# Kernel optimization log

Hardware: AMD Instinct MI355X
Metric: run time of the kernel (lower is better)

The kernel has to match this reference:

```python
import jax, jax.numpy as jnp
import numpy as np

L, B, D_IN, LATENT, H_ODE = 50, 256, 256, 512, 1024
DT = 0.1  # uniform time increment per observation


def setup_inputs() -> dict:
    key = jax.random.key(0)
    ks = jax.random.split(key, 9)
    feat = jax.random.normal(ks[0], (L, B, D_IN), dtype=jnp.float32)
    tp = jnp.full((L, B, 1), DT, dtype=jnp.float32)
    data = jnp.concatenate([feat, tp], axis=-1)  # (L, B, D_IN+1)
    hid = 2 * LATENT  # GRUCell hidden size
    s_mlp1 = 1.0 / np.sqrt(LATENT)
    s_mlp2 = 1.0 / np.sqrt(H_ODE)
    s_gru_i = 1.0 / np.sqrt(hid)
    return {
        "data": data,
        # ODE func MLP: Linear(LATENT,H_ODE) -> tanh -> Linear(H_ODE,LATENT)
        "mlp_w1": jax.random.uniform(ks[1], (LATENT, H_ODE), jnp.float32, -s_mlp1, s_mlp1),
        "mlp_b1": jax.random.uniform(ks[2], (H_ODE,), jnp.float32, -s_mlp1, s_mlp1),
        "mlp_w2": jax.random.uniform(ks[3], (H_ODE, LATENT), jnp.float32, -s_mlp2, s_mlp2),
        "mlp_b2": jax.random.uniform(ks[4], (LATENT,), jnp.float32, -s_mlp2, s_mlp2),
        # GRUCell(D_IN, hid): torch layout W_ih (3*hid, D_IN), W_hh (3*hid, hid)
        "gru_wih": jax.random.uniform(ks[5], (3 * hid, D_IN), jnp.float32, -s_gru_i, s_gru_i),
        "gru_bih": jax.random.uniform(ks[6], (3 * hid,), jnp.float32, -s_gru_i, s_gru_i),
        "gru_whh": jax.random.uniform(ks[7], (3 * hid, hid), jnp.float32, -s_gru_i, s_gru_i),
        "gru_bhh": jax.random.uniform(ks[8], (3 * hid,), jnp.float32, -s_gru_i, s_gru_i),
    }


def reference(data, mlp_w1, mlp_b1, mlp_w2, mlp_b2, gru_wih, gru_bih, gru_whh, gru_bhh):
    x_seq = data[..., :-1]          # (L, B, D_IN)
    dt_seq = data[..., -1]          # (L, B) per-step time increments
    l, bs, _ = x_seq.shape
    latent = mlp_w1.shape[0]

    # With uniform dt, minimum_step = total/200 and each step uses
    # n_intermediate_tp = floor(200/L) linspace points -> n_sub Euler substeps.
    n_tp = max(2, 200 // l)
    n_sub = n_tp - 1

    def ode_f(y):
        return jnp.tanh(y @ mlp_w1 + mlp_b1) @ mlp_w2 + mlp_b2

    def gru_cell(x, h):
        gi = x @ gru_wih.T + gru_bih
        gh = h @ gru_whh.T + gru_bhh
        ir, iz, inn = jnp.split(gi, 3, axis=-1)
        hr, hz, hn = jnp.split(gh, 3, axis=-1)
        r = jax.nn.sigmoid(ir + hr)
        z = jax.nn.sigmoid(iz + hz)
        n = jnp.tanh(inn + r * hn)
        return (1.0 - z) * n + z * h

    def step(carry, inp):
        ode_state, gru_state, _ = carry
        x, dt = inp                      # x: (B, D_IN), dt: (B,)
        h_step = (dt / n_sub)[:, None]   # Euler substep size
        y = ode_state
        for _ in range(n_sub):           # fixed small unroll
            y = y + ode_f(y) * h_step
        new_h = gru_cell(x, jnp.concatenate([y, gru_state], axis=-1))
        # Original code: ode_state = new_h[..., :latent]; gru_state = new_h[..., :-latent]
        # (both are the first `latent` dims -- faithful to the source)
        new_ode = new_h[:, :latent]
        new_gru = new_h[:, :latent]
        return (new_ode, new_gru, new_h), new_ode

    zeros_lat = jnp.zeros((bs, latent), dtype=data.dtype)
    init = (zeros_lat, zeros_lat, jnp.zeros((bs, 2 * latent), dtype=data.dtype))
    (_, _, new_h), ode_states_post = jax.lax.scan(step, init, (x_seq, dt_seq))
    return ode_states_post, new_h
```

## Files before the change

kernel.cpp:

```cpp
#include <hip/hip_runtime.h>

#define LSEQ 50
#define BATCH 256
#define DIN 256
#define LAT 512
#define HID 1024
#define ROWSTRIDE 257
#define NBLK 256

typedef __attribute__((ext_vector_type(8))) short s16x8;
typedef __attribute__((ext_vector_type(4))) float f32x4;
using u16 = unsigned short;
using u64 = unsigned long long;

__device__ __forceinline__ u16 bfhi(float v) {
  union { float f; unsigned u; } a; a.f = v;
  return (u16)((a.u + 0x7FFFu + ((a.u >> 16) & 1u)) >> 16);
}
__device__ __forceinline__ void split2(float v, u16& h, u16& l) {
  u16 hu = bfhi(v);
  union { unsigned u; float f; } hf; hf.u = ((unsigned)hu) << 16;
  h = hu; l = bfhi(v - hf.f);
}
__device__ __forceinline__ float p2f(u16 h, u16 l) {
  union { unsigned u; float f; } a, b;
  a.u = ((unsigned)h) << 16; b.u = ((unsigned)l) << 16;
  return a.f + b.f;
}
__device__ __forceinline__ float sigmoidf_(float x) { return 1.f / (1.f + __expf(-x)); }
__device__ __forceinline__ f32x4 mfma16(s16x8 a, s16x8 b, f32x4 c) {
  return __builtin_amdgcn_mfma_f32_16x16x32_bf16(a, b, c, 0, 0, 0);
}
__device__ __forceinline__ ushort4 ldu4(const u16* p) { return *(const ushort4*)p; }
__device__ __forceinline__ void stu4(u16* p, ushort4 v) { *(ushort4*)p = v; }

__device__ __forceinline__ ushort4 ldu4c(const u16* p) {
  u64 v = __hip_atomic_load((const u64*)p, __ATOMIC_RELAXED, __HIP_MEMORY_SCOPE_AGENT);
  union { u64 q; ushort4 s; } u; u.q = v; return u.s;
}
__device__ __forceinline__ u16 ldu16c(const u16* p) {
  return __hip_atomic_load(p, __ATOMIC_RELAXED, __HIP_MEMORY_SCOPE_AGENT);
}
__device__ __forceinline__ void stu16c(u16* p, u16 v) {
  __hip_atomic_store(p, v, __ATOMIC_RELAXED, __HIP_MEMORY_SCOPE_AGENT);
}

__device__ __forceinline__ void slice_barrier(unsigned* line, unsigned k) {
  asm volatile("s_waitcnt vmcnt(0)" ::: "memory");
  __syncthreads();
  if (threadIdx.x == 0) {
    __hip_atomic_fetch_add(line, 1u, __ATOMIC_RELAXED, __HIP_MEMORY_SCOPE_AGENT);
    const unsigned tgt = k * 32u;
    while (__hip_atomic_load(line, __ATOMIC_RELAXED, __HIP_MEMORY_SCOPE_AGENT) < tgt) {
      __builtin_amdgcn_s_sleep(1);
    }
  }
  __syncthreads();
}

__global__ __launch_bounds__(256) void tsplit_k(const float* __restrict__ W,
    u16* __restrict__ Thi, u16* __restrict__ Tlo, int K, int N)
{
  __shared__ unsigned Ts[32][33];
  const int bk = blockIdx.x * 32, bn = blockIdx.y * 32;
  const int t = threadIdx.x;
  const int n_l = t & 31, k_l4 = (t >> 5) * 4;
  #pragma unroll
  for (int i = 0; i < 4; i++) {
    float v = W[(size_t)(bk + k_l4 + i) * N + bn + n_l];
    u16 h, l; split2(v, h, l);
    Ts[k_l4 + i][n_l] = ((unsigned)h << 16) | l;
  }
  __syncthreads();
  const int k_l = t & 31, n_l2 = t >> 5;
  #pragma unroll
  for (int i = 0; i < 4; i++) {
    int nn = n_l2 + 8 * i;
    unsigned u = Ts[k_l][nn];
    size_t o = (size_t)(bn + nn) * K + bk + k_l;
    Thi[o] = (u16)(u >> 16);
    Tlo[o] = (u16)(u & 0xFFFFu);
  }
}

__global__ __launch_bounds__(256) void esplit_k(const float* __restrict__ W,
    u16* __restrict__ Phi, u16* __restrict__ Plo)
{
  size_t i4 = ((size_t)blockIdx.x * 256 + threadIdx.x) * 4;
  float4 v = *(const float4*)&W[i4];
  u16 h[4], l[4];
  split2(v.x, h[0], l[0]); split2(v.y, h[1], l[1]);
  split2(v.z, h[2], l[2]); split2(v.w, h[3], l[3]);
  *(ushort4*)&Phi[i4] = make_ushort4(h[0], h[1], h[2], h[3]);
  *(ushort4*)&Plo[i4] = make_ushort4(l[0], l[1], l[2], l[3]);
}

__global__ __launch_bounds__(256) void init_k(u16* __restrict__ c0h, u16* __restrict__ c0l,
                                              unsigned* __restrict__ bar)
{
  size_t i4 = ((size_t)blockIdx.x * 256 + threadIdx.x) * 4;
  *(ushort4*)&c0h[i4] = make_ushort4(0, 0, 0, 0);
  *(ushort4*)&c0l[i4] = make_ushort4(0, 0, 0, 0);
  if (blockIdx.x == 0 && threadIdx.x < 16) bar[threadIdx.x * 64] = 0u;
}

template<int EPI, int NITER>
__device__ __forceinline__ void gemm_phase(
    u16* __restrict__ Sah, u16* __restrict__ Sal,
    u16* __restrict__ Sbh, u16* __restrict__ Sbl,
    const u16* __restrict__ Ahi, const u16* __restrict__ Alo, int ldA, int m0,
    const u16* __restrict__ Bhi, const u16* __restrict__ Blo, int ldB, int n0,
    const float* __restrict__ bias,
    u16* __restrict__ Ohi, u16* __restrict__ Olo,
    const float* __restrict__ data, int t, int tid)
{
  const int lane = tid & 63, wave = tid >> 6;
  const int wm = (wave >> 1) << 4, wn = (wave & 1) << 4;
  const int lr = lane & 15, lq = lane >> 4;
  const int srow = tid >> 3, sk4 = (tid & 7) << 2;
  const int sidx = srow * 40 + sk4;
  const size_t rowA = (size_t)(m0 + srow) * ldA + sk4;
  const size_t rowB = (size_t)(n0 + srow) * ldB + sk4;
  f32x4 acc = {0.f, 0.f, 0.f, 0.f};
  ushort4 rah[4], ral[4], rbh[4], rbl[4];
  #pragma unroll
  for (int d = 0; d < 4; ++d) {
    const int k0 = d << 5;
    rah[d] = ldu4c(&Ahi[rowA + k0]); ral[d] = ldu4c(&Alo[rowA + k0]);
    rbh[d] = ldu4(&Bhi[rowB + k0]);  rbl[d] = ldu4(&Blo[rowB + k0]);
  }
  #pragma unroll
  for (int d = 0; d < 4; ++d) {
    stu4(&Sah[d * 1280 + sidx], rah[d]); stu4(&Sal[d * 1280 + sidx], ral[d]);
    stu4(&Sbh[d * 1280 + sidx], rbh[d]); stu4(&Sbl[d * 1280 + sidx], rbl[d]);
  }
  __syncthreads();
  constexpr int NSEG = NITER / 4;
  for (int p = 0; p < NSEG; ++p) {
    const int rb = (p & 1) * 5120;
    const int wb = 5120 - rb;
    const bool pf = (p + 1 < NSEG);
    if (pf) {
      #pragma unroll
      for (int d = 0; d < 4; ++d) {
        const int k0 = (((p + 1) << 2) + d) << 5;
        rah[d] = ldu4c(&Ahi[rowA + k0]); ral[d] = ldu4c(&Alo[rowA + k0]);
        rbh[d] = ldu4(&Bhi[rowB + k0]);  rbl[d] = ldu4(&Blo[rowB + k0]);
      }
    }
    #pragma unroll
    for (int d = 0; d < 4; ++d) {
      const int fa = rb + d * 1280 + (wm + lr) * 40 + lq * 8;
      const int fb = rb + d * 1280 + (wn + lr) * 40 + lq * 8;
      s16x8 ah = *(const s16x8*)&Sah[fa];
      s16x8 al = *(const s16x8*)&Sal[fa];
      s16x8 bh = *(const s16x8*)&Sbh[fb];
      s16x8 bl = *(const s16x8*)&Sbl[fb];
      acc = mfma16(ah, bh, acc);
      acc = mfma16(ah, bl, acc);
      acc = mfma16(al, bh, acc);
    }
    if (pf) {
      #pragma unroll
      for (int d = 0; d < 4; ++d) {
        stu4(&Sah[wb + d * 1280 + sidx], rah[d]); stu4(&Sal[wb + d * 1280 + sidx], ral[d]);
        stu4(&Sbh[wb + d * 1280 + sidx], rbh[d]); stu4(&Sbl[wb + d * 1280 + sidx], rbl[d]);
      }
    }
    __syncthreads();
  }
  #pragma unroll
  for (int r = 0; r < 4; ++r) {
    const int row = m0 + wm + lq * 4 + r;
    const int col = n0 + wn + lr;
    float v = acc[r] + bias[col];
    size_t o = (size_t)row * HID + col;
    if (EPI == 1) {
      float h1 = tanhf(v);
      u16 h, l; split2(h1, h, l);
      stu16c(&Ohi[o], h); stu16c(&Olo[o], l);
    } else {
      float dt3 = data[(size_t)(t * BATCH + row) * ROWSTRIDE + DIN] * (1.f / 3.f);
      float y = p2f(ldu16c(&Ohi[o]), ldu16c(&Olo[o])) + v * dt3;
      u16 h, l; split2(y, h, l);
      stu16c(&Ohi[o], h); stu16c(&Olo[o], l);
    }
  }
}

template<bool PLANES>
__device__ __forceinline__ void gru_phase(
    u16* pool,
    const u16* __restrict__ chi, const u16* __restrict__ clo,
    const float* __restrict__ whh, const u16* __restrict__ whhh, const u16* __restrict__ whhl,
    const float* __restrict__ wih, const u16* __restrict__ wihh, const u16* __restrict__ wihl,
    const float* __restrict__ bih, const float* __restrict__ bhh,
    const float* __restrict__ data, int t,
    u16* __restrict__ nhi, u16* __restrict__ nlo,
    float* __restrict__ out, int g0, int m0, int tid)
{
  u16* sAh = pool;
  u16* sAl = pool + 5120;
  u16* sBh = pool + 10240;
  u16* sBl = pool + 25600;
  const int lane = tid & 63, wave = tid >> 6;
  const int wm = (wave >> 1) << 4, wn = (wave & 1) << 4;
  const int lr = lane & 15, lq = lane >> 4;
  const int srow = tid >> 3, sk4 = (tid & 7) << 2;
  const int sidx = srow * 40 + sk4;
  f32x4 aR = {0,0,0,0}, aZ = {0,0,0,0}, aNh = {0,0,0,0}, aNi = {0,0,0,0};

  ushort4 rah[2], ral[2], rbh[2][3], rbl[2][3];
  float4  rbf[2][3];
  float   rxf[2][4];

  {
    const size_t rowA = (size_t)(m0 + srow) * HID + sk4;
    #pragma unroll
    for (int j = 0; j < 2; ++j) {
      const int k0 = j << 5;
      rah[j] = ldu4c(&chi[rowA + k0]); ral[j] = ldu4c(&clo[rowA + k0]);
      #pragma unroll
      for (int g = 0; g < 3; ++g) {
        const size_t rr = (size_t)(g * 1024 + g0 + srow) * 1024 + k0 + sk4;
        if (PLANES) { rbh[j][g] = ldu4(&whhh[rr]); rbl[j][g] = ldu4(&whhl[rr]); }
        else rbf[j][g] = *(const float4*)&whh[rr];
      }
    }
    #pragma unroll
    for (int j = 0; j < 2; ++j) {
      stu4(&sAh[j * 1280 + sidx], rah[j]); stu4(&sAl[j * 1280 + sidx], ral[j]);
      #pragma unroll
      for (int g = 0; g < 3; ++g) {
        if (PLANES) {
          stu4(&sBh[j * 3840 + g * 1280 + sidx], rbh[j][g]);
          stu4(&sBl[j * 3840 + g * 1280 + sidx], rbl[j][g]);
        } else {
          float4 w4 = rbf[j][g];
          u16 h0,l0,h1,l1,h2,l2,h3,l3;
          split2(w4.x,h0,l0); split2(w4.y,h1,l1); split2(w4.z,h2,l2); split2(w4.w,h3,l3);
          stu4(&sBh[j * 3840 + g * 1280 + sidx], make_ushort4(h0,h1,h2,h3));
          stu4(&sBl[j * 3840 + g * 1280 + sidx], make_ushort4(l0,l1,l2,l3));
        }
      }
    }
    __syncthreads();
    for (int p = 0; p < 16; ++p) {
      const int rb = (p & 1) * 2;
      const int wb = 2 - rb;
      const bool pf = (p + 1 < 16);
      if (pf) {
        #pragma unroll
        for (int j = 0; j < 2; ++j) {
          const int k0 = (((p + 1) << 1) + j) << 5;
          rah[j] = ldu4c(&chi[rowA + k0]); ral[j] = ldu4c(&clo[rowA + k0]);
          #pragma unroll
          for (int g = 0; g < 3; ++g) {
            const size_t rr = (size_t)(g * 1024 + g0 + srow) * 1024 + k0 + sk4;
            if (PLANES) { rbh[j][g] = ldu4(&whhh[rr]); rbl[j][g] = ldu4(&whhl[rr]); }
            else rbf[j][g] = *(const float4*)&whh[rr];
          }
        }
      }
      #pragma unroll
      for (int j = 0; j < 2; ++j) {
        const int sa = (rb + j) * 1280 + (wm + lr) * 40 + lq * 8;
        const int sb = (rb + j) * 3840 + (wn + lr) * 40 + lq * 8;
        s16x8 ah = *(const s16x8*)&sAh[sa];
        s16x8 al = *(const s16x8*)&sAl[sa];
        #pragma unroll
        for (int g = 0; g < 3; ++g) {
          s16x8 bh = *(const s16x8*)&sBh[sb + g * 1280];
          s16x8 bl = *(const s16x8*)&sBl[sb + g * 1280];
          f32x4 c = (g == 0) ? aR : (g == 1) ? aZ : aNh;
          c = mfma16(ah, bh, c); c = mfma16(ah, bl, c); c = mfma16(al, bh, c);
          if (g == 0) aR = c; else if (g == 1) aZ = c; else aNh = c;
        }
      }
      if (pf) {
        #pragma unroll
        for (int j = 0; j < 2; ++j) {
          stu4(&sAh[(wb + j) * 1280 + sidx], rah[j]); stu4(&sAl[(wb + j) * 1280 + sidx], ral[j]);
          #pragma unroll
          for (int g = 0; g < 3; ++g) {
            if (PLANES) {
              stu4(&sBh[(wb + j) * 3840 + g * 1280 + sidx], rbh[j][g]);
              stu4(&sBl[(wb + j) * 3840 + g * 1280 + sidx], rbl[j][g]);
            } else {
              float4 w4 = rbf[j][g];
              u16 h0,l0,h1,l1,h2,l2,h3,l3;
              split2(w4.x,h0,l0); split2(w4.y,h1,l1); split2(w4.z,h2,l2); split2(w4.w,h3,l3);
              stu4(&sBh[(wb + j) * 3840 + g * 1280 + sidx], make_ushort4(h0,h1,h2,h3));
              stu4(&sBl[(wb + j) * 3840 + g * 1280 + sidx], make_ushort4(l0,l1,l2,l3));
            }
          }
        }
      }
      __syncthreads();
    }
  }

  {
    const size_t rowX = (size_t)(t * BATCH + m0 + srow) * ROWSTRIDE + sk4;
    #pragma unroll
    for (int j = 0; j < 2; ++j) {
      const int k0 = j << 5;
      #pragma unroll
      for (int i = 0; i < 4; ++i) rxf[j][i] = data[rowX + k0 + i];
      #pragma unroll
      for (int g = 0; g < 3; ++g) {
        const size_t rr = (size_t)(g * 1024 + g0 + srow) * 256 + k0 + sk4;
        if (PLANES) { rbh[j][g] = ldu4(&wihh[rr]); rbl[j][g] = ldu4(&wihl[rr]); }
        else rbf[j][g] = *(const float4*)&wih[rr];
      }
    }
    #pragma unroll
    for (int j = 0; j < 2; ++j) {
      u16 xh[4], xl[4];
      #pragma unroll
      for (int i = 0; i < 4; ++i) split2(rxf[j][i], xh[i], xl[i]);
      stu4(&sAh[j * 1280 + sidx], make_ushort4(xh[0], xh[1], xh[2], xh[3]));
      stu4(&sAl[j * 1280 + sidx], make_ushort4(xl[0], xl[1], xl[2], xl[3]));
      #pragma unroll
      for (int g = 0; g < 3; ++g) {
        if (PLANES) {
          stu4(&sBh[j * 3840 + g * 1280 + sidx], rbh[j][g]);
          stu4(&sBl[j * 3840 + g * 1280 + sidx], rbl[j][g]);
        } else {
          float4 w4 = rbf[j][g];
          u16 h0,l0,h1,l1,h2,l2,h3,l3;
          split2(w4.x,h0,l0); split2(w4.y,h1,l1); split2(w4.z,h2,l2); split2(w4.w,h3,l3);
          stu4(&sBh[j * 3840 + g * 1280 + sidx], make_ushort4(h0,h1,h2,h3));
          stu4(&sBl[j * 3840 + g * 1280 + sidx], make_ushort4(l0,l1,l2,l3));
        }
      }
    }
    __syncthreads();
    for (int p = 0; p < 4; ++p) {
      const int rb = (p & 1) * 2;
      const int wb = 2 - rb;
      const bool pf = (p + 1 < 4);
      if (pf) {
        #pragma unroll
        for (int j = 0; j < 2; ++j) {
          const int k0 = (((p + 1) << 1) + j) << 5;
          #pragma unroll
          for (int i = 0; i < 4; ++i) rxf[j][i] = data[rowX + k0 + i];
          #pragma unroll
          for (int g = 0; g < 3; ++g) {
            const size_t rr = (size_t)(g * 1024 + g0 + srow) * 256 + k0 + sk4;
            if (PLANES) { rbh[j][g] = ldu4(&wihh[rr]); rbl[j][g] = ldu4(&wihl[rr]); }
            else rbf[j][g] = *(const float4*)&wih[rr];
          }
        }
      }
      #pragma unroll
      for (int j = 0; j < 2; ++j) {
        const int sa = (rb + j) * 1280 + (wm + lr) * 40 + lq * 8;
        const int sb = (rb + j) * 3840 + (wn + lr) * 40 + lq * 8;
        s16x8 ah = *(const s16x8*)&sAh[sa];
        s16x8 al = *(const s16x8*)&sAl[sa];
        #pragma unroll
        for (int g = 0; g < 3; ++g) {
          s16x8 bh = *(const s16x8*)&sBh[sb + g * 1280];
          s16x8 bl = *(const s16x8*)&sBl[sb + g * 1280];
          f32x4 c = (g == 0) ? aR : (g == 1) ? aZ : aNi;
          c = mfma16(ah, bh, c); c = mfma16(ah, bl, c); c = mfma16(al, bh, c);
          if (g == 0) aR = c; else if (g == 1) aZ = c; else aNi = c;
        }
      }
      if (pf) {
        #pragma unroll
        for (int j = 0; j < 2; ++j) {
          u16 xh[4], xl[4];
          #pragma unroll
          for (int i = 0; i < 4; ++i) split2(rxf[j][i], xh[i], xl[i]);
          stu4(&sAh[(wb + j) * 1280 + sidx], make_ushort4(xh[0], xh[1], xh[2], xh[3]));
          stu4(&sAl[(wb + j) * 1280 + sidx], make_ushort4(xl[0], xl[1], xl[2], xl[3]));
          #pragma unroll
          for (int g = 0; g < 3; ++g) {
            if (PLANES) {
              stu4(&sBh[(wb + j) * 3840 + g * 1280 + sidx], rbh[j][g]);
              stu4(&sBl[(wb + j) * 3840 + g * 1280 + sidx], rbl[j][g]);
            } else {
              float4 w4 = rbf[j][g];
              u16 h0,l0,h1,l1,h2,l2,h3,l3;
              split2(w4.x,h0,l0); split2(w4.y,h1,l1); split2(w4.z,h2,l2); split2(w4.w,h3,l3);
              stu4(&sBh[(wb + j) * 3840 + g * 1280 + sidx], make_ushort4(h0,h1,h2,h3));
              stu4(&sBl[(wb + j) * 3840 + g * 1280 + sidx], make_ushort4(l0,l1,l2,l3));
            }
          }
        }
      }
      __syncthreads();
    }
  }

  #pragma unroll
  for (int r = 0; r < 4; ++r) {
    const int row = m0 + wm + lq * 4 + r;
    const int jg = g0 + wn + lr;
    float rr = sigmoidf_(aR[r] + bih[jg] + bhh[jg]);
    float zz = sigmoidf_(aZ[r] + bih[1024 + jg] + bhh[1024 + jg]);
    float nn = tanhf(aNi[r] + bih[2048 + jg] + rr * (aNh[r] + bhh[2048 + jg]));
    size_t oh = (size_t)row * HID + jg;
    float hv = p2f(ldu16c(&chi[oh]), ldu16c(&clo[oh]));
    float val = (1.f - zz) * nn + zz * hv;
    out[(size_t)LSEQ * BATCH * LAT + oh] = val;
    if (jg < LAT) {
      out[((size_t)t * BATCH + row) * LAT + jg] = val;
      u16 h, l; split2(val, h, l);
      stu16c(&nhi[oh], h); stu16c(&nhi[oh + LAT], h);
      stu16c(&nlo[oh], l); stu16c(&nlo[oh + LAT], l);
    }
  }
}

template<bool PLANES>
__global__ __launch_bounds__(256, 1) void fused_seq_k(
    const u16* __restrict__ w1h, const u16* __restrict__ w1l,
    const u16* __restrict__ w2h, const u16* __restrict__ w2l,
    const float* __restrict__ b1, const float* __restrict__ b2,
    u16* __restrict__ c0h, u16* __restrict__ c0l,
    u16* __restrict__ c1h, u16* __restrict__ c1l,
    u16* __restrict__ h1h, u16* __restrict__ h1l,
    const float* __restrict__ whh, const u16* __restrict__ whhh, const u16* __restrict__ whhl,
    const float* __restrict__ wih, const u16* __restrict__ wihh, const u16* __restrict__ wihl,
    const float* __restrict__ bih, const float* __restrict__ bhh,
    const float* __restrict__ data, float* __restrict__ out,
    unsigned* __restrict__ bar)
{
  __shared__ u16 pool[40960];
  const int b = blockIdx.x;
  const int tid = threadIdx.x;
  const int slice = b >> 5;
  const int l = b & 31;
  const int m0 = slice << 5;
  unsigned* line = bar + slice * 64;
  unsigned rnd = 0;

  u16* Sah = pool;
  u16* Sal = pool + 10240;
  u16* Sbh = pool + 20480;
  u16* Sbl = pool + 30720;

  for (int t = 0; t < LSEQ; ++t) {
    u16* chi = (t & 1) ? c1h : c0h;
    u16* clo = (t & 1) ? c1l : c0l;
    u16* nhi = (t & 1) ? c0h : c1h;
    u16* nlo = (t & 1) ? c0l : c1l;
    for (int s = 0; s < 3; ++s) {
      {
        const int n0 = l << 5;
        gemm_phase<1, 16>(Sah, Sal, Sbh, Sbl,
                          chi, clo, HID, m0, w1h, w1l, 512, n0,
                          b1, h1h, h1l, data, t, tid);
      }
      ++rnd; slice_barrier(line, rnd);
      if (l < 16) {
        const int n0 = l << 5;
        gemm_phase<2, 32>(Sah, Sal, Sbh, Sbl,
                          h1h, h1l, HID, m0, w2h, w2l, 1024, n0,
                          b2, chi, clo, data, t, tid);
      }
      ++rnd; slice_barrier(line, rnd);
    }
    gru_phase<PLANES>(pool, chi, clo, whh, whhh, whhl, wih, wihh, wihl,
                      bih, bhh, data, t, nhi, nlo, out, l << 5, m0, tid);
    if (t + 1 < LSEQ) { ++rnd; slice_barrier(line, rnd); }
  }
}

extern "C" void kernel_launch(void* const* d_in, const int* in_sizes, int n_in,
                              void* d_out, int out_size, void* d_ws, size_t ws_size,
                              hipStream_t stream)
{
  const float* data = (const float*)d_in[0];
  const float* w1   = (const float*)d_in[1];
  const float* b1   = (const float*)d_in[2];
  const float* w2   = (const float*)d_in[3];
  const float* b2   = (const float*)d_in[4];
  const float* wih  = (const float*)d_in[5];
  const float* bih  = (const float*)d_in[6];
  const float* whh  = (const float*)d_in[7];
  const float* bhh  = (const float*)d_in[8];
  float* out = (float*)d_out;

  char* w = (char*)d_ws;
  auto alloc = [&](size_t bytes) { char* p = w; w += bytes; return p; };
  u16* w1h = (u16*)alloc((size_t)512 * 1024 * 2);
  u16* w1l = (u16*)alloc((size_t)512 * 1024 * 2);
  u16* w2h = (u16*)alloc((size_t)512 * 1024 * 2);
  u16* w2l = (u16*)alloc((size_t)512 * 1024 * 2);
  u16* c0h = (u16*)alloc((size_t)BATCH * HID * 2);
  u16* c0l = (u16*)alloc((size_t)BATCH * HID * 2);
  u16* c1h = (u16*)alloc((size_t)BATCH * HID * 2);
  u16* c1l = (u16*)alloc((size_t)BATCH * HID * 2);
  u16* h1h = (u16*)alloc((size_t)BATCH * HID * 2);
  u16* h1l = (u16*)alloc((size_t)BATCH * HID * 2);
  unsigned* bar = (unsigned*)alloc(4096);
  size_t base = (size_t)(w - (char*)d_ws);
  size_t need_opt = base + 2 * ((size_t)3072 * 1024 * 2) + 2 * ((size_t)3072 * 256 * 2);
  bool planes = ws_size >= need_opt;
  u16 *whhh = nullptr, *whhl = nullptr, *wihh = nullptr, *wihl = nullptr;
  if (planes) {
    whhh = (u16*)alloc((size_t)3072 * 1024 * 2);
    whhl = (u16*)alloc((size_t)3072 * 1024 * 2);
    wihh = (u16*)alloc((size_t)3072 * 256 * 2);
    wihl = (u16*)alloc((size_t)3072 * 256 * 2);
  }

  tsplit_k<<<dim3(512 / 32, 1024 / 32), 256, 0, stream>>>(w1, w1h, w1l, 512, 1024);
  tsplit_k<<<dim3(1024 / 32, 512 / 32), 256, 0, stream>>>(w2, w2h, w2l, 1024, 512);
  if (planes) {
    esplit_k<<<dim3((3072 * 1024) / 1024), 256, 0, stream>>>(whh, whhh, whhl);
    esplit_k<<<dim3((3072 * 256) / 1024), 256, 0, stream>>>(wih, wihh, wihl);
  }
  init_k<<<dim3(256), 256, 0, stream>>>(c0h, c0l, bar);

  if (planes) {
    fused_seq_k<true><<<dim3(NBLK), dim3(256), 0, stream>>>(
        w1h, w1l, w2h, w2l, b1, b2, c0h, c0l, c1h, c1l, h1h, h1l,
        whh, whhh, whhl, wih, wihh, wihl, bih, bhh, data, out, bar);
  } else {
    fused_seq_k<false><<<dim3(NBLK), dim3(256), 0, stream>>>(
        w1h, w1l, w2h, w2l, b1, b2, c0h, c0l, c1h, c1l, h1h, h1l,
        whh, whhh, whhl, wih, wihh, wihl, bih, bhh, data, out, bar);
  }
}
```

Before: 3.921 ms.

## Restructure GEMM and GRU k-loops into explicit two-stage register/LDS pipeline

Rewrites the K loops in the GEMM and GRU phases as an explicit ping-pong pipeline. Two register sets are filled from global memory while the other LDS buffer is being computed, and the loops are unrolled by two. __syncthreads is replaced by an lgkmcnt wait plus s_barrier, which avoids draining outstanding global loads at every barrier. Accumulators are also split into two independent chains to shorten MFMA dependency stalls, and launch_bounds drops the min-blocks hint. The cost is higher register pressure and more code.

```diff
diff --git a/kernel.cpp b/kernel.cpp
--- a/kernel.cpp
+++ b/kernel.cpp
@@ -31,6 +31,9 @@
 __device__ __forceinline__ f32x4 mfma16(s16x8 a, s16x8 b, f32x4 c) {
   return __builtin_amdgcn_mfma_f32_16x16x32_bf16(a, b, c, 0, 0, 0);
 }
+__device__ __forceinline__ f32x4 mfma3(s16x8 ah, s16x8 al, s16x8 bh, s16x8 bl, f32x4 c) {
+  c = mfma16(ah, bh, c); c = mfma16(ah, bl, c); c = mfma16(al, bh, c); return c;
+}
 __device__ __forceinline__ ushort4 ldu4(const u16* p) { return *(const ushort4*)p; }
 __device__ __forceinline__ void stu4(u16* p, ushort4 v) { *(ushort4*)p = v; }
 
@@ -43,6 +46,11 @@
 }
 __device__ __forceinline__ void stu16c(u16* p, u16 v) {
   __hip_atomic_store(p, v, __ATOMIC_RELAXED, __HIP_MEMORY_SCOPE_AGENT);
+}
+
+__device__ __forceinline__ void kbar() {
+  asm volatile("s_waitcnt lgkmcnt(0)" ::: "memory");
+  __builtin_amdgcn_s_barrier();
 }
 
 __device__ __forceinline__ void slice_barrier(unsigned* line, unsigned k) {
@@ -114,6 +122,7 @@
     u16* __restrict__ Ohi, u16* __restrict__ Olo,
     const float* __restrict__ data, int t, int tid)
 {
+  constexpr int NSEG = NITER / 4;
   const int lane = tid & 63, wave = tid >> 6;
   const int wm = (wave >> 1) << 4, wn = (wave & 1) << 4;
   const int lr = lane & 15, lq = lane >> 4;
@@ -121,59 +130,76 @@
   const int sidx = srow * 40 + sk4;
   const size_t rowA = (size_t)(m0 + srow) * ldA + sk4;
   const size_t rowB = (size_t)(n0 + srow) * ldB + sk4;
-  f32x4 acc = {0.f, 0.f, 0.f, 0.f};
-  ushort4 rah[4], ral[4], rbh[4], rbl[4];
-  #pragma unroll
-  for (int d = 0; d < 4; ++d) {
-    const int k0 = d << 5;
-    rah[d] = ldu4c(&Ahi[rowA + k0]); ral[d] = ldu4c(&Alo[rowA + k0]);
-    rbh[d] = ldu4(&Bhi[rowB + k0]);  rbl[d] = ldu4(&Blo[rowB + k0]);
-  }
-  #pragma unroll
-  for (int d = 0; d < 4; ++d) {
-    stu4(&Sah[d * 1280 + sidx], rah[d]); stu4(&Sal[d * 1280 + sidx], ral[d]);
-    stu4(&Sbh[d * 1280 + sidx], rbh[d]); stu4(&Sbl[d * 1280 + sidx], rbl[d]);
-  }
-  __syncthreads();
-  constexpr int NSEG = NITER / 4;
-  for (int p = 0; p < NSEG; ++p) {
-    const int rb = (p & 1) * 5120;
-    const int wb = 5120 - rb;
-    const bool pf = (p + 1 < NSEG);
-    if (pf) {
-      #pragma unroll
-      for (int d = 0; d < 4; ++d) {
-        const int k0 = (((p + 1) << 2) + d) << 5;
-        rah[d] = ldu4c(&Ahi[rowA + k0]); ral[d] = ldu4c(&Alo[rowA + k0]);
-        rbh[d] = ldu4(&Bhi[rowB + k0]);  rbl[d] = ldu4(&Blo[rowB + k0]);
-      }
-    }
+  const int fa = (wm + lr) * 40 + lq * 8;
+  const int fb = (wn + lr) * 40 + lq * 8;
+  f32x4 acc0 = {0,0,0,0}, acc1 = {0,0,0,0};
+
+  ushort4 ah0[4], al0[4], bh0[4], bl0[4];
+  ushort4 ah1[4], al1[4], bh1[4], bl1[4];
+
+  auto load0 = [&](int seg) {
     #pragma unroll
     for (int d = 0; d < 4; ++d) {
-      const int fa = rb + d * 1280 + (wm + lr) * 40 + lq * 8;
-      const int fb = rb + d * 1280 + (wn + lr) * 40 + lq * 8;
-      s16x8 ah = *(const s16x8*)&Sah[fa];
-      s16x8 al = *(const s16x8*)&Sal[fa];
-      s16x8 bh = *(const s16x8*)&Sbh[fb];
-      s16x8 bl = *(const s16x8*)&Sbl[fb];
-      acc = mfma16(ah, bh, acc);
-      acc = mfma16(ah, bl, acc);
-      acc = mfma16(al, bh, acc);
-    }
-    if (pf) {
-      #pragma unroll
-      for (int d = 0; d < 4; ++d) {
-        stu4(&Sah[wb + d * 1280 + sidx], rah[d]); stu4(&Sal[wb + d * 1280 + sidx], ral[d]);
-        stu4(&Sbh[wb + d * 1280 + sidx], rbh[d]); stu4(&Sbl[wb + d * 1280 + sidx], rbl[d]);
-      }
-    }
-    __syncthreads();
-  }
+      const int k0 = (seg * 4 + d) << 5;
+      ah0[d] = ldu4c(&Ahi[rowA + k0]); al0[d] = ldu4c(&Alo[rowA + k0]);
+      bh0[d] = ldu4(&Bhi[rowB + k0]);  bl0[d] = ldu4(&Blo[rowB + k0]);
+    }
+  };
+  auto load1 = [&](int seg) {
+    #pragma unroll
+    for (int d = 0; d < 4; ++d) {
+      const int k0 = (seg * 4 + d) << 5;
+      ah1[d] = ldu4c(&Ahi[rowA + k0]); al1[d] = ldu4c(&Alo[rowA + k0]);
+      bh1[d] = ldu4(&Bhi[rowB + k0]);  bl1[d] = ldu4(&Blo[rowB + k0]);
+    }
+  };
+  auto write0 = [&]() {
+    #pragma unroll
+    for (int d = 0; d < 4; ++d) {
+      stu4(&Sah[d * 1280 + sidx], ah0[d]); stu4(&Sal[d * 1280 + sidx], al0[d]);
+      stu4(&Sbh[d * 1280 + sidx], bh0[d]); stu4(&Sbl[d * 1280 + sidx], bl0[d]);
+    }
+  };
+  auto write1 = [&]() {
+    #pragma unroll
+    for (int d = 0; d < 4; ++d) {
+      stu4(&Sah[5120 + d * 1280 + sidx], ah1[d]); stu4(&Sal[5120 + d * 1280 + sidx], al1[d]);
+      stu4(&Sbh[5120 + d * 1280 + sidx], bh1[d]); stu4(&Sbl[5120 + d * 1280 + sidx], bl1[d]);
+    }
+  };
+  auto compute = [&](int g) {
+    #pragma unroll
+    for (int d = 0; d < 4; ++d) {
+      const int o = g * 5120 + d * 1280;
+      s16x8 ah = *(const s16x8*)&Sah[o + fa];
+      s16x8 al = *(const s16x8*)&Sal[o + fa];
+      s16x8 bh = *(const s16x8*)&Sbh[o + fb];
+      s16x8 bl = *(const s16x8*)&Sbl[o + fb];
+      if (d & 1) acc1 = mfma3(ah, al, bh, bl, acc1);
+      else       acc0 = mfma3(ah, al, bh, bl, acc0);
+    }
+  };
+
+  load0(0);
+  load1(1);
+  write0();
+  kbar();
+  for (int p = 0; p < NSEG; p += 2) {
+    if (p + 2 < NSEG) load0(p + 2);
+    compute(0);
+    write1();
+    kbar();
+    if (p + 3 < NSEG) load1(p + 3);
+    compute(1);
+    if (p + 2 < NSEG) write0();
+    kbar();
+  }
+
   #pragma unroll
   for (int r = 0; r < 4; ++r) {
     const int row = m0 + wm + lq * 4 + r;
     const int col = n0 + wn + lr;
-    float v = acc[r] + bias[col];
+    float v = acc0[r] + acc1[r] + bias[col];
     size_t o = (size_t)row * HID + col;
     if (EPI == 1) {
       float h1 = tanhf(v);
@@ -197,7 +223,7 @@
     const float* __restrict__ bih, const float* __restrict__ bhh,
     const float* __restrict__ data, int t,
     u16* __restrict__ nhi, u16* __restrict__ nlo,
-    float* __restrict__ out, int g0, int m0, int tid)
+    float* __restrict__ out, int gc0, int m0, int tid)
 {
   u16* sAh = pool;
   u16* sAl = pool + 5120;
@@ -208,198 +234,261 @@
   const int lr = lane & 15, lq = lane >> 4;
   const int srow = tid >> 3, sk4 = (tid & 7) << 2;
   const int sidx = srow * 40 + sk4;
-  f32x4 aR = {0,0,0,0}, aZ = {0,0,0,0}, aNh = {0,0,0,0}, aNi = {0,0,0,0};
-
-  ushort4 rah[2], ral[2], rbh[2][3], rbl[2][3];
-  float4  rbf[2][3];
-  float   rxf[2][4];
+  const int fa = (wm + lr) * 40 + lq * 8;
+  const int fbn = (wn + lr) * 40 + lq * 8;
+  f32x4 aR0 = {0,0,0,0}, aR1 = {0,0,0,0};
+  f32x4 aZ0 = {0,0,0,0}, aZ1 = {0,0,0,0};
+  f32x4 aNh0 = {0,0,0,0}, aNh1 = {0,0,0,0};
+  f32x4 aNi0 = {0,0,0,0}, aNi1 = {0,0,0,0};
 
   {
     const size_t rowA = (size_t)(m0 + srow) * HID + sk4;
-    #pragma unroll
-    for (int j = 0; j < 2; ++j) {
-      const int k0 = j << 5;
-      rah[j] = ldu4c(&chi[rowA + k0]); ral[j] = ldu4c(&clo[rowA + k0]);
-      #pragma unroll
-      for (int g = 0; g < 3; ++g) {
-        const size_t rr = (size_t)(g * 1024 + g0 + srow) * 1024 + k0 + sk4;
-        if (PLANES) { rbh[j][g] = ldu4(&whhh[rr]); rbl[j][g] = ldu4(&whhl[rr]); }
-        else rbf[j][g] = *(const float4*)&whh[rr];
-      }
-    }
-    #pragma unroll
-    for (int j = 0; j < 2; ++j) {
-      stu4(&sAh[j * 1280 + sidx], rah[j]); stu4(&sAl[j * 1280 + sidx], ral[j]);
-      #pragma unroll
-      for (int g = 0; g < 3; ++g) {
+    const size_t rB0 = (size_t)(0 * 1024 + gc0 + srow) * 1024 + sk4;
+    const size_t rB1 = (size_t)(1 * 1024 + gc0 + srow) * 1024 + sk4;
+    const size_t rB2 = (size_t)(2 * 1024 + gc0 + srow) * 1024 + sk4;
+    ushort4 Ah0[2], Al0[2], Bh0[2][3], Bl0[2][3];
+    ushort4 Ah1[2], Al1[2], Bh1[2][3], Bl1[2][3];
+    float4  F0[2][3], F1[2][3];
+
+    auto load0 = [&](int seg) {
+      #pragma unroll
+      for (int j = 0; j < 2; ++j) {
+        const int k0 = (seg * 2 + j) << 5;
+        Ah0[j] = ldu4c(&chi[rowA + k0]); Al0[j] = ldu4c(&clo[rowA + k0]);
         if (PLANES) {
-          stu4(&sBh[j * 3840 + g * 1280 + sidx], rbh[j][g]);
-          stu4(&sBl[j * 3840 + g * 1280 + sidx], rbl[j][g]);
+          Bh0[j][0] = ldu4(&whhh[rB0 + k0]); Bl0[j][0] = ldu4(&whhl[rB0 + k0]);
+          Bh0[j][1] = ldu4(&whhh[rB1 + k0]); Bl0[j][1] = ldu4(&whhl[rB1 + k0]);
+          Bh0[j][2] = ldu4(&whhh[rB2 + k0]); Bl0[j][2] = ldu4(&whhl[rB2 + k0]);
         } else {
-          float4 w4 = rbf[j][g];
-          u16 h0,l0,h1,l1,h2,l2,h3,l3;
-          split2(w4.x,h0,l0); split2(w4.y,h1,l1); split2(w4.z,h2,l2); split2(w4.w,h3,l3);
-          stu4(&sBh[j * 3840 + g * 1280 + sidx], make_ushort4(h0,h1,h2,h3));
-          stu4(&sBl[j * 3840 + g * 1280 + sidx], make_ushort4(l0,l1,l2,l3));
-        }
-      }
-    }
-    __syncthreads();
-    for (int p = 0; p < 16; ++p) {
-      const int rb = (p & 1) * 2;
-      const int wb = 2 - rb;
-      const bool pf = (p + 1 < 16);
-      if (pf) {
+          F0[j][0] = *(const float4*)&whh[rB0 + k0];
+          F0[j][1] = *(const float4*)&whh[rB1 + k0];
+          F0[j][2] = *(const float4*)&whh[rB2 + k0];
+        }
+      }
+    };
+    auto load1 = [&](int seg) {
+      #pragma unroll
+      for (int j = 0; j < 2; ++j) {
+        const int k0 = (seg * 2 + j) << 5;
+        Ah1[j] = ldu4c(&chi[rowA + k0]); Al1[j] = ldu4c(&clo[rowA + k0]);
+        if (PLANES) {
+          Bh1[j][0] = ldu4(&whhh[rB0 + k0]); Bl1[j][0] = ldu4(&whhl[rB0 + k0]);
+          Bh1[j][1] = ldu4(&whhh[rB1 + k0]); Bl1[j][1] = ldu4(&whhl[rB1 + k0]);
+          Bh1[j][2] = ldu4(&whhh[rB2 + k0]); Bl1[j][2] = ldu4(&whhl[rB2 + k0]);
+        } else {
+          F1[j][0] = *(const float4*)&whh[rB0 + k0];
+          F1[j][1] = *(const float4*)&whh[rB1 + k0];
+          F1[j][2] = *(const float4*)&whh[rB2 + k0];
+        }
+      }
+    };
+    auto write0 = [&]() {
+      #pragma unroll
+      for (int j = 0; j < 2; ++j) {
+        stu4(&sAh[j * 1280 + sidx], Ah0[j]); stu4(&sAl[j * 1280 + sidx], Al0[j]);
         #pragma unroll
-        for (int j = 0; j < 2; ++j) {
-          const int k0 = (((p + 1) << 1) + j) << 5;
-          rah[j] = ldu4c(&chi[rowA + k0]); ral[j] = ldu4c(&clo[rowA + k0]);
-          #pragma unroll
-          for (int g = 0; g < 3; ++g) {
-            const size_t rr = (size_t)(g * 1024 + g0 + srow) * 1024 + k0 + sk4;
-            if (PLANES) { rbh[j][g] = ldu4(&whhh[rr]); rbl[j][g] = ldu4(&whhl[rr]); }
-            else rbf[j][g] = *(const float4*)&whh[rr];
+        for (int g = 0; g < 3; ++g) {
+          if (PLANES) {
+            stu4(&sBh[j * 3840 + g * 1280 + sidx], Bh0[j][g]);
+            stu4(&sBl[j * 3840 + g * 1280 + sidx], Bl0[j][g]);
+          } else {
+            float4 w4 = F0[j][g];
+            u16 h0,l0,h1,l1,h2,l2,h3,l3;
+            split2(w4.x,h0,l0); split2(w4.y,h1,l1); split2(w4.z,h2,l2); split2(w4.w,h3,l3);
+            stu4(&sBh[j * 3840 + g * 1280 + sidx], make_ushort4(h0,h1,h2,h3));
+            stu4(&sBl[j * 3840 + g * 1280 + sidx], make_ushort4(l0,l1,l2,l3));
           }
         }
       }
-      #pragma unroll
-      for (int j = 0; j < 2; ++j) {
-        const int sa = (rb + j) * 1280 + (wm + lr) * 40 + lq * 8;
-        const int sb = (rb + j) * 3840 + (wn + lr) * 40 + lq * 8;
+    };
+    auto write1 = [&]() {
+      #pragma unroll
+      for (int j = 0; j < 2; ++j) {
+        stu4(&sAh[(2 + j) * 1280 + sidx], Ah1[j]); stu4(&sAl[(2 + j) * 1280 + sidx], Al1[j]);
+        #pragma unroll
+        for (int g = 0; g < 3; ++g) {
+          if (PLANES) {
+            stu4(&sBh[(2 + j) * 3840 + g * 1280 + sidx], Bh1[j][g]);
+            stu4(&sBl[(2 + j) * 3840 + g * 1280 + sidx], Bl1[j][g]);
+          } else {
+            float4 w4 = F1[j][g];
+            u16 h0,l0,h1,l1,h2,l2,h3,l3;
+            split2(w4.x,h0,l0); split2(w4.y,h1,l1); split2(w4.z,h2,l2); split2(w4.w,h3,l3);
+            stu4(&sBh[(2 + j) * 3840 + g * 1280 + sidx], make_ushort4(h0,h1,h2,h3));
+            stu4(&sBl[(2 + j) * 3840 + g * 1280 + sidx], make_ushort4(l0,l1,l2,l3));
+          }
+        }
+      }
+    };
+    auto compute = [&](int grp) {
+      #pragma unroll
+      for (int j = 0; j < 2; ++j) {
+        const int slot = grp * 2 + j;
+        const int sa = slot * 1280 + fa;
+        const int sb = slot * 3840 + fbn;
         s16x8 ah = *(const s16x8*)&sAh[sa];
         s16x8 al = *(const s16x8*)&sAl[sa];
         #pragma unroll
         for (int g = 0; g < 3; ++g) {
           s16x8 bh = *(const s16x8*)&sBh[sb + g * 1280];
           s16x8 bl = *(const s16x8*)&sBl[sb + g * 1280];
-          f32x4 c = (g == 0) ? aR : (g == 1) ? aZ : aNh;
-          c = mfma16(ah, bh, c); c = mfma16(ah, bl, c); c = mfma16(al, bh, c);
-          if (g == 0) aR = c; else if (g == 1) aZ = c; else aNh = c;
-        }
-      }
-      if (pf) {
-        #pragma unroll
-        for (int j = 0; j < 2; ++j) {
-          stu4(&sAh[(wb + j) * 1280 + sidx], rah[j]); stu4(&sAl[(wb + j) * 1280 + sidx], ral[j]);
-          #pragma unroll
-          for (int g = 0; g < 3; ++g) {
-            if (PLANES) {
-              stu4(&sBh[(wb + j) * 3840 + g * 1280 + sidx], rbh[j][g]);
-              stu4(&sBl[(wb + j) * 3840 + g * 1280 + sidx], rbl[j][g]);
-            } else {
-              float4 w4 = rbf[j][g];
-              u16 h0,l0,h1,l1,h2,l2,h3,l3;
-              split2(w4.x,h0,l0); split2(w4.y,h1,l1); split2(w4.z,h2,l2); split2(w4.w,h3,l3);
-              stu4(&sBh[(wb + j) * 3840 + g * 1280 + sidx], make_ushort4(h0,h1,h2,h3));
-              stu4(&sBl[(wb + j) * 3840 + g * 1280 + sidx], make_ushort4(l0,l1,l2,l3));
-            }
+          if (j) {
+            if (g == 0) aR1 = mfma3(ah, al, bh, bl, aR1);
+            else if (g == 1) aZ1 = mfma3(ah, al, bh, bl, aZ1);
+            else aNh1 = mfma3(ah, al, bh, bl, aNh1);
+          } else {
+            if (g == 0) aR0 = mfma3(ah, al, bh, bl, aR0);
+            else if (g == 1) aZ0 = mfma3(ah, al, bh, bl, aZ0);
+            else aNh0 = mfma3(ah, al, bh, bl, aNh0);
           }
         }
       }
-      __syncthreads();
+    };
+
+    load0(0); load1(1); write0(); kbar();
+    for (int p = 0; p < 16; p += 2) {
+      if (p + 2 < 16) load0(p + 2);
+      compute(0);
+      write1();
+      kbar();
+      if (p + 3 < 16) load1(p + 3);
+      compute(1);
+      if (p + 2 < 16) write0();
+      kbar();
     }
   }
 
   {
     const size_t rowX = (size_t)(t * BATCH + m0 + srow) * ROWSTRIDE + sk4;
-    #pragma unroll
-    for (int j = 0; j < 2; ++j) {
-      const int k0 = j << 5;
-      #pragma unroll
-      for (int i = 0; i < 4; ++i) rxf[j][i] = data[rowX + k0 + i];
-      #pragma unroll
-      for (int g = 0; g < 3; ++g) {
-        const size_t rr = (size_t)(g * 1024 + g0 + srow) * 256 + k0 + sk4;
-        if (PLANES) { rbh[j][g] = ldu4(&wihh[rr]); rbl[j][g] = ldu4(&wihl[rr]); }
-        else rbf[j][g] = *(const float4*)&wih[rr];
-      }
-    }
-    #pragma unroll
-    for (int j = 0; j < 2; ++j) {
-      u16 xh[4], xl[4];
-      #pragma unroll
-      for (int i = 0; i < 4; ++i) split2(rxf[j][i], xh[i], xl[i]);
-      stu4(&sAh[j * 1280 + sidx], make_ushort4(xh[0], xh[1], xh[2], xh[3]));
-      stu4(&sAl[j * 1280 + sidx], make_ushort4(xl[0], xl[1], xl[2], xl[3]));
-      #pragma unroll
-      for (int g = 0; g < 3; ++g) {
+    const size_t rB0 = (size_t)(0 * 1024 + gc0 + srow) * 256 + sk4;
+    const size_t rB1 = (size_t)(1 * 1024 + gc0 + srow) * 256 + sk4;
+    const size_t rB2 = (size_t)(2 * 1024 + gc0 + srow) * 256 + sk4;
+    float4  X0[2], X1[2];
+    ushort4 Bh0[2][3], Bl0[2][3], Bh1[2][3], Bl1[2][3];
+    float4  F0[2][3], F1[2][3];
+
+    auto load0 = [&](int seg) {
+      #pragma unroll
+      for (int j = 0; j < 2; ++j) {
+        const int k0 = (seg * 2 + j) << 5;
+        X0[j] = *(const float4*)&data[rowX + k0];
         if (PLANES) {
-          stu4(&sBh[j * 3840 + g * 1280 + sidx], rbh[j][g]);
-          stu4(&sBl[j * 3840 + g * 1280 + sidx], rbl[j][g]);
+          Bh0[j][0] = ldu4(&wihh[rB0 + k0]); Bl0[j][0] = ldu4(&wihl[rB0 + k0]);
+          Bh0[j][1] = ldu4(&wihh[rB1 + k0]); Bl0[j][1] = ldu4(&wihl[rB1 + k0]);
+          Bh0[j][2] = ldu4(&wihh[rB2 + k0]); Bl0[j][2] = ldu4(&wihl[rB2 + k0]);
         } else {
-          float4 w4 = rbf[j][g];
-          u16 h0,l0,h1,l1,h2,l2,h3,l3;
-          split2(w4.x,h0,l0); split2(w4.y,h1,l1); split2(w4.z,h2,l2); split2(w4.w,h3,l3);
-          stu4(&sBh[j * 3840 + g * 1280 + sidx], make_ushort4(h0,h1,h2,h3));
-          stu4(&sBl[j * 3840 + g * 1280 + sidx], make_ushort4(l0,l1,l2,l3));
-        }
-      }
-    }
-    __syncthreads();
-    for (int p = 0; p < 4; ++p) {
-      const int rb = (p & 1) * 2;
-      const int wb = 2 - rb;
-      const bool pf = (p + 1 < 4);
-      if (pf) {
+          F0[j][0] = *(const float4*)&wih[rB0 + k0];
+          F0[j][1] = *(const float4*)&wih[rB1 + k0];
+          F0[j][2] = *(const float4*)&wih[rB2 + k0];
+        }
+      }
+    };
+    auto load1 = [&](int seg) {
+      #pragma unroll
+      for (int j = 0; j < 2; ++j) {
+        const int k0 = (seg * 2 + j) << 5;
+        X1[j] = *(const float4*)&data[rowX + k0];
+        if (PLANES) {
+          Bh1[j][0] = ldu4(&wihh[rB0 + k0]); Bl1[j][0] = ldu4(&wihl[rB0 + k0]);
+          Bh1[j][1] = ldu4(&wihh[rB1 + k0]); Bl1[j][1] = ldu4(&wihl[rB1 + k0]);
+          Bh1[j][2] = ldu4(&wihh[rB2 + k0]); Bl1[j][2] = ldu4(&wihl[rB2 + k0]);
+        } else {
+          F1[j][0] = *(const float4*)&wih[rB0 + k0];
+          F1[j][1] = *(const float4*)&wih[rB1 + k0];
+          F1[j][2] = *(const float4*)&wih[rB2 + k0];
+        }
+      }
+    };
+    auto writeX = [&](const float4* X, int base) {
+      #pragma unroll
+      for (int j = 0; j < 2; ++j) {
+        u16 xh[4], xl[4];
+        split2(X[j].x, xh[0], xl[0]); split2(X[j].y, xh[1], xl[1]);
+        split2(X[j].z, xh[2], xl[2]); split2(X[j].w, xh[3], xl[3]);
+        stu4(&sAh[(base + j) * 1280 + sidx], make_ushort4(xh[0], xh[1], xh[2], xh[3]));
+        stu4(&sAl[(base + j) * 1280 + sidx], make_ushort4(xl[0], xl[1], xl[2], xl[3]));
+      }
+    };
+    auto write0 = [&]() {
+      writeX(X0, 0);
+      #pragma unroll
+      for (int j = 0; j < 2; ++j)
         #pragma unroll
-        for (int j = 0; j < 2; ++j) {
-          const int k0 = (((p + 1) << 1) + j) << 5;
-          #pragma unroll
-          for (int i = 0; i < 4; ++i) rxf[j][i] = data[rowX + k0 + i];
-          #pragma unroll
-          for (int g = 0; g < 3; ++g) {
-            const size_t rr = (size_t)(g * 1024 + g0 + srow) * 256 + k0 + sk4;
-            if (PLANES) { rbh[j][g] = ldu4(&wihh[rr]); rbl[j][g] = ldu4(&wihl[rr]); }
-            else rbf[j][g] = *(const float4*)&wih[rr];
+        for (int g = 0; g < 3; ++g) {
+          if (PLANES) {
+            stu4(&sBh[j * 3840 + g * 1280 + sidx], Bh0[j][g]);
+            stu4(&sBl[j * 3840 + g * 1280 + sidx], Bl0[j][g]);
+          } else {
+            float4 w4 = F0[j][g];
+            u16 h0,l0,h1,l1,h2,l2,h3,l3;
+            split2(w4.x,h0,l0); split2(w4.y,h1,l1); split2(w4.z,h2,l2); split2(w4.w,h3,l3);
+            stu4(&sBh[j * 3840 + g * 1280 + sidx], make_ushort4(h0,h1,h2,h3));
+            stu4(&sBl[j * 3840 + g * 1280 + sidx], make_ushort4(l0,l1,l2,l3));
           }
         }
-      }
-      #pragma unroll
-      for (int j = 0; j < 2; ++j) {
-        const int sa = (rb + j) * 1280 + (wm + lr) * 40 + lq * 8;
-        const int sb = (rb + j) * 3840 + (wn + lr) * 40 + lq * 8;
+    };
+    auto write1 = [&]() {
+      writeX(X1, 2);
+      #pragma unroll
+      for (int j = 0; j < 2; ++j)
+        #pragma unroll
+        for (int g = 0; g < 3; ++g) {
+          if (PLANES) {
+            stu4(&sBh[(2 + j) * 3840 + g * 1280 + sidx], Bh1[j][g]);
+            stu4(&sBl[(2 + j) * 3840 + g * 1280 + sidx], Bl1[j][g]);
+          } else {
+            float4 w4 = F1[j][g];
+            u16 h0,l0,h1,l1,h2,l2,h3,l3;
+            split2(w4.x,h0,l0); split2(w4.y,h1,l1); split2(w4.z,h2,l2); split2(w4.w,h3,l3);
+            stu4(&sBh[(2 + j) * 3840 + g * 1280 + sidx], make_ushort4(h0,h1,h2,h3));
+            stu4(&sBl[(2 + j) * 3840 + g * 1280 + sidx], make_ushort4(l0,l1,l2,l3));
+          }
+        }
+    };
+    auto compute = [&](int grp) {
+      #pragma unroll
+      for (int j = 0; j < 2; ++j) {
+        const int slot = grp * 2 + j;
+        const int sa = slot * 1280 + fa;
+        const int sb = slot * 3840 + fbn;
         s16x8 ah = *(const s16x8*)&sAh[sa];
         s16x8 al = *(const s16x8*)&sAl[sa];
         #pragma unroll
         for (int g = 0; g < 3; ++g) {
           s16x8 bh = *(const s16x8*)&sBh[sb + g * 1280];
           s16x8 bl = *(const s16x8*)&sBl[sb + g * 1280];
-          f32x4 c = (g == 0) ? aR : (g == 1) ? aZ : aNi;
-          c = mfma16(ah, bh, c); c = mfma16(ah, bl, c); c = mfma16(al, bh, c);
-          if (g == 0) aR = c; else if (g == 1) aZ = c; else aNi = c;
-        }
-      }
-      if (pf) {
-        #pragma unroll
-        for (int j = 0; j < 2; ++j) {
-          u16 xh[4], xl[4];
-          #pragma unroll
-          for (int i = 0; i < 4; ++i) split2(rxf[j][i], xh[i], xl[i]);
-          stu4(&sAh[(wb + j) * 1280 + sidx], make_ushort4(xh[0], xh[1], xh[2], xh[3]));
-          stu4(&sAl[(wb + j) * 1280 + sidx], make_ushort4(xl[0], xl[1], xl[2], xl[3]));
-          #pragma unroll
-          for (int g = 0; g < 3; ++g) {
-            if (PLANES) {
-              stu4(&sBh[(wb + j) * 3840 + g * 1280 + sidx], rbh[j][g]);
-              stu4(&sBl[(wb + j) * 3840 + g * 1280 + sidx], rbl[j][g]);
-            } else {
-              float4 w4 = rbf[j][g];
-              u16 h0,l0,h1,l1,h2,l2,h3,l3;
-              split2(w4.x,h0,l0); split2(w4.y,h1,l1); split2(w4.z,h2,l2); split2(w4.w,h3,l3);
-              stu4(&sBh[(wb + j) * 3840 + g * 1280 + sidx], make_ushort4(h0,h1,h2,h3));
-              stu4(&sBl[(wb + j) * 3840 + g * 1280 + sidx], make_ushort4(l0,l1,l2,l3));
-            }
+          if (j) {
+            if (g == 0) aR1 = mfma3(ah, al, bh, bl, aR1);
+            else if (g == 1) aZ1 = mfma3(ah, al, bh, bl, aZ1);
+            else aNi1 = mfma3(ah, al, bh, bl, aNi1);
+          } else {
+            if (g == 0) aR0 = mfma3(ah, al, bh, bl, aR0);
+            else if (g == 1) aZ0 = mfma3(ah, al, bh, bl, aZ0);
+            else aNi0 = mfma3(ah, al, bh, bl, aNi0);
           }
         }
       }
-      __syncthreads();
-    }
-  }
+    };
+
+    load0(0); load1(1); write0(); kbar();
+    for (int p = 0; p < 4; p += 2) {
+      if (p + 2 < 4) load0(p + 2);
+      compute(0);
+      write1();
+      kbar();
+      if (p + 3 < 4) load1(p + 3);
+      compute(1);
+      if (p + 2 < 4) write0();
+      kbar();
+    }
+  }
+
+  const f32x4 aR = aR0 + aR1, aZ = aZ0 + aZ1, aNh = aNh0 + aNh1, aNi = aNi0 + aNi1;
 
   #pragma unroll
   for (int r = 0; r < 4; ++r) {
     const int row = m0 + wm + lq * 4 + r;
-    const int jg = g0 + wn + lr;
+    const int jg = gc0 + wn + lr;
     float rr = sigmoidf_(aR[r] + bih[jg] + bhh[jg]);
     float zz = sigmoidf_(aZ[r] + bih[1024 + jg] + bhh[1024 + jg]);
     float nn = tanhf(aNi[r] + bih[2048 + jg] + rr * (aNh[r] + bhh[2048 + jg]));
@@ -417,7 +506,7 @@
 }
 
 template<bool PLANES>
-__global__ __launch_bounds__(256, 1) void fused_seq_k(
+__global__ __launch_bounds__(256) void fused_seq_k(
     const u16* __restrict__ w1h, const u16* __restrict__ w1l,
     const u16* __restrict__ w2h, const u16* __restrict__ w2l,
     const float* __restrict__ b1, const float* __restrict__ b2,
```

Measured after the change: 4.000 ms. +2.0%, slower.
